# Kernel optimization log

Hardware: AMD Instinct MI355X
Metric: run time of the kernel (lower is better)

Reference implementation:

```python
import jax, jax.numpy as jnp
import numpy as np

NUM_EXPERTS = 8
NUM_FEATURES = 2048


def setup_inputs() -> dict:
    key = jax.random.key(0)
    k1, k2, k3 = jax.random.split(key, 3)
    hidden_states = jax.random.normal(k1, (8192, NUM_FEATURES), dtype=jnp.float32)
    gate_up_proj = jax.random.normal(k2, (NUM_EXPERTS, NUM_FEATURES, 2 * NUM_FEATURES), dtype=jnp.float32)
    down_proj = jax.random.normal(k3, (NUM_EXPERTS, NUM_FEATURES, NUM_FEATURES), dtype=jnp.float32)
    return {"hidden_states": hidden_states, "gate_up_proj": gate_up_proj, "down_proj": down_proj}


def reference(hidden_states, gate_up_proj, down_proj):
    E, D = gate_up_proj.shape[0], gate_up_proj.shape[1]
    # (E, T, D) tokens pre-sorted per expert
    h = hidden_states.reshape(E, -1, D)
    # per-expert batched GEMM: (E, T, 2D)
    gate_up = jnp.einsum('etd,edf->etf', h, gate_up_proj)
    gate, up = gate_up[..., :D], gate_up[..., D:]
    # ReLU-gated activation, then down projection: (E, T, D)
    out = jnp.einsum('etd,edf->etf', up * jax.nn.relu(gate), down_proj)
    return out.reshape(-1, D)
```

## Files before the change

### kernel.cpp

```cpp
#include <hip/hip_runtime.h>
#include <stdint.h>


#define NEXP 8
#define DIM  2048
#define TOK  1024
#define NGU  4096
#define BM   128
#define BN   128
#define BK   32
#define LDST 40

typedef __attribute__((ext_vector_type(8))) short short8;
typedef __attribute__((ext_vector_type(4))) float f32x4;

__device__ __forceinline__ uint32_t pkbf(float lo, float hi) {
  return __builtin_amdgcn_perm(__float_as_uint(hi) + 0x8000u,
                               __float_as_uint(lo) + 0x8000u, 0x07060302u);
}

__device__ __forceinline__ uint16_t bf16_rne(float x) {
  uint32_t u = __float_as_uint(x);
  return (uint16_t)((u + 0x7fffu + ((u >> 16) & 1u)) >> 16);
}

__global__ __launch_bounds__(256, 2) void k_gateup(const float* __restrict__ H,
                                                   const float* __restrict__ W1,
                                                   uint16_t* __restrict__ ACT) {
  __shared__ uint16_t As[BM * LDST];
  __shared__ uint16_t Bg[BN * LDST];
  __shared__ uint16_t Bu[BN * LDST];

  const int tid = threadIdx.x;
  const int e   = blockIdx.z;
  const int m0  = blockIdx.y * BM;
  const int n0  = blockIdx.x * BN;

  const float* hA = H + (size_t)(e * TOK + m0) * DIM;
  const float* wE = W1 + (size_t)e * DIM * NGU;

  const int ar = tid >> 1;
  const int ak = (tid & 1) << 4;
  const float* aptr = hA + (size_t)ar * DIM + ak;
  uint16_t* asw = &As[ar * LDST + ak];

  const int bn = tid & 127;
  const int bk = (tid >> 7) << 4;
  const float* gptr = wE + (size_t)bk * NGU + (n0 + bn);
  const float* uptr = gptr + DIM;
  uint16_t* bgw = &Bg[bn * LDST + bk];
  uint16_t* buw = &Bu[bn * LDST + bk];

  const int lane = tid & 63;
  const int wid  = tid >> 6;
  const int wr = (wid >> 1) << 6;
  const int wc = (wid & 1) << 6;
  const int lm = lane & 15;
  const int qd = lane >> 4;

  f32x4 accg[4][4], accu[4][4];
  const f32x4 zero = {0.f, 0.f, 0.f, 0.f};
#pragma unroll
  for (int i = 0; i < 4; ++i)
#pragma unroll
    for (int j = 0; j < 4; ++j) { accg[i][j] = zero; accu[i][j] = zero; }

  const uint16_t* afr = &As[(wr + lm) * LDST + (qd << 3)];
  const uint16_t* gfr = &Bg[(wc + lm) * LDST + (qd << 3)];
  const uint16_t* ufr = &Bu[(wc + lm) * LDST + (qd << 3)];

  for (int k0 = 0; k0 < DIM; k0 += BK) {
    float4 a0 = *(const float4*)(aptr + 0);
    float4 a1 = *(const float4*)(aptr + 4);
    float4 a2 = *(const float4*)(aptr + 8);
    float4 a3 = *(const float4*)(aptr + 12);
    uint4 aw0 = make_uint4(pkbf(a0.x, a0.y), pkbf(a0.z, a0.w),
                           pkbf(a1.x, a1.y), pkbf(a1.z, a1.w));
    uint4 aw1 = make_uint4(pkbf(a2.x, a2.y), pkbf(a2.z, a2.w),
                           pkbf(a3.x, a3.y), pkbf(a3.z, a3.w));

    float g[16], u[16];
#pragma unroll
    for (int i = 0; i < 16; ++i) g[i] = gptr[(size_t)i * NGU];
#pragma unroll
    for (int i = 0; i < 16; ++i) u[i] = uptr[(size_t)i * NGU];
    uint4 gw0 = make_uint4(pkbf(g[0], g[1]),  pkbf(g[2], g[3]),
                           pkbf(g[4], g[5]),  pkbf(g[6], g[7]));
    uint4 gw1 = make_uint4(pkbf(g[8], g[9]),  pkbf(g[10], g[11]),
                           pkbf(g[12], g[13]), pkbf(g[14], g[15]));
    uint4 uw0 = make_uint4(pkbf(u[0], u[1]),  pkbf(u[2], u[3]),
                           pkbf(u[4], u[5]),  pkbf(u[6], u[7]));
    uint4 uw1 = make_uint4(pkbf(u[8], u[9]),  pkbf(u[10], u[11]),
                           pkbf(u[12], u[13]), pkbf(u[14], u[15]));

    __syncthreads();
    *(uint4*)(asw)     = aw0;
    *(uint4*)(asw + 8) = aw1;
    *(uint4*)(bgw)     = gw0;
    *(uint4*)(bgw + 8) = gw1;
    *(uint4*)(buw)     = uw0;
    *(uint4*)(buw + 8) = uw1;
    __syncthreads();

    short8 a[4], bgf[4], buf[4];
#pragma unroll
    for (int i = 0; i < 4; ++i) a[i] = *(const short8*)(afr + i * 16 * LDST);
#pragma unroll
    for (int j = 0; j < 4; ++j) {
      bgf[j] = *(const short8*)(gfr + j * 16 * LDST);
      buf[j] = *(const short8*)(ufr + j * 16 * LDST);
    }
#pragma unroll
    for (int i = 0; i < 4; ++i)
#pragma unroll
      for (int j = 0; j < 4; ++j) {
        accg[i][j] = __builtin_amdgcn_mfma_f32_16x16x32_bf16(a[i], bgf[j], accg[i][j], 0, 0, 0);
        accu[i][j] = __builtin_amdgcn_mfma_f32_16x16x32_bf16(a[i], buf[j], accu[i][j], 0, 0, 0);
      }

    aptr += BK;
    gptr += (size_t)BK * NGU;
    uptr += (size_t)BK * NGU;
  }

  uint16_t* actE = ACT + (size_t)(e * TOK + m0) * DIM + n0;
#pragma unroll
  for (int i = 0; i < 4; ++i)
#pragma unroll
    for (int j = 0; j < 4; ++j)
#pragma unroll
      for (int t = 0; t < 4; ++t) {
        int row = wr + i * 16 + qd * 4 + t;
        int col = wc + j * 16 + lm;
        float gv = accg[i][j][t];
        float uv = accu[i][j][t];
        actE[(size_t)row * DIM + col] = bf16_rne(uv * fmaxf(gv, 0.f));
      }
}

__global__ __launch_bounds__(256, 3) void k_down(const uint16_t* __restrict__ ACT,
                                                 const float* __restrict__ W2,
                                                 float* __restrict__ OUT) {
  __shared__ uint16_t As[BM * LDST];
  __shared__ uint16_t Bs[BN * LDST];

  const int tid = threadIdx.x;
  const int e   = blockIdx.z;
  const int m0  = blockIdx.y * BM;
  const int n0  = blockIdx.x * BN;

  const uint16_t* aA = ACT + (size_t)(e * TOK + m0) * DIM;
  const float* wE = W2 + (size_t)e * DIM * DIM;

  const int ar = tid >> 1;
  const int ak = (tid & 1) << 4;
  const uint16_t* aptr = aA + (size_t)ar * DIM + ak;
  uint16_t* asw = &As[ar * LDST + ak];

  const int bn = tid & 127;
  const int bk = (tid >> 7) << 4;
  const float* bptr = wE + (size_t)bk * DIM + (n0 + bn);
  uint16_t* bsw = &Bs[bn * LDST + bk];

  const int lane = tid & 63;
  const int wid  = tid >> 6;
  const int wr = (wid >> 1) << 6;
  const int wc = (wid & 1) << 6;
  const int lm = lane & 15;
  const int qd = lane >> 4;

  f32x4 acc[4][4];
  const f32x4 zero = {0.f, 0.f, 0.f, 0.f};
#pragma unroll
  for (int i = 0; i < 4; ++i)
#pragma unroll
    for (int j = 0; j < 4; ++j) acc[i][j] = zero;

  const uint16_t* afr = &As[(wr + lm) * LDST + (qd << 3)];
  const uint16_t* bfr = &Bs[(wc + lm) * LDST + (qd << 3)];

  for (int k0 = 0; k0 < DIM; k0 += BK) {
    uint4 aw0 = *(const uint4*)(aptr);
    uint4 aw1 = *(const uint4*)(aptr + 8);
    float b[16];
#pragma unroll
    for (int i = 0; i < 16; ++i) b[i] = bptr[(size_t)i * DIM];
    uint4 bw0 = make_uint4(pkbf(b[0], b[1]),  pkbf(b[2], b[3]),
                           pkbf(b[4], b[5]),  pkbf(b[6], b[7]));
    uint4 bw1 = make_uint4(pkbf(b[8], b[9]),  pkbf(b[10], b[11]),
                           pkbf(b[12], b[13]), pkbf(b[14], b[15]));

    __syncthreads();
    *(uint4*)(asw)     = aw0;
    *(uint4*)(asw + 8) = aw1;
    *(uint4*)(bsw)     = bw0;
    *(uint4*)(bsw + 8) = bw1;
    __syncthreads();

    short8 a[4], bf[4];
#pragma unroll
    for (int i = 0; i < 4; ++i) a[i] = *(const short8*)(afr + i * 16 * LDST);
#pragma unroll
    for (int j = 0; j < 4; ++j) bf[j] = *(const short8*)(bfr + j * 16 * LDST);
#pragma unroll
    for (int i = 0; i < 4; ++i)
#pragma unroll
      for (int j = 0; j < 4; ++j)
        acc[i][j] = __builtin_amdgcn_mfma_f32_16x16x32_bf16(a[i], bf[j], acc[i][j], 0, 0, 0);

    aptr += BK;
    bptr += (size_t)BK * DIM;
  }

  float* outE = OUT + (size_t)(e * TOK + m0) * DIM + n0;
#pragma unroll
  for (int i = 0; i < 4; ++i)
#pragma unroll
    for (int j = 0; j < 4; ++j)
#pragma unroll
      for (int t = 0; t < 4; ++t) {
        int row = wr + i * 16 + qd * 4 + t;
        int col = wc + j * 16 + lm;
        outE[(size_t)row * DIM + col] = acc[i][j][t];
      }
}

extern "C" void kernel_launch(void* const* d_in, const int* in_sizes, int n_in,
                              void* d_out, int out_size, void* d_ws, size_t ws_size,
                              hipStream_t stream) {
  const float* H  = (const float*)d_in[0];
  const float* W1 = (const float*)d_in[1];
  const float* W2 = (const float*)d_in[2];
  float* OUT = (float*)d_out;
  uint16_t* ACT = (uint16_t*)d_ws;

  dim3 blk(256);
  dim3 g1(DIM / BN, TOK / BM, NEXP);
  k_gateup<<<g1, blk, 0, stream>>>(H, W1, ACT);
  dim3 g2(DIM / BN, TOK / BM, NEXP);
  k_down<<<g2, blk, 0, stream>>>(ACT, W2, OUT);
}
```

Measured before the change: 785.7 us.

## Prefetch next K-tile into registers and load down-proj A fragments directly from global

```diff
diff --git a/kernel.cpp b/kernel.cpp
--- a/kernel.cpp
+++ b/kernel.cpp
@@ -69,21 +69,22 @@
   const uint16_t* gfr = &Bg[(wc + lm) * LDST + (qd << 3)];
   const uint16_t* ufr = &Bu[(wc + lm) * LDST + (qd << 3)];
 
+  float4 a0 = *(const float4*)(aptr + 0);
+  float4 a1 = *(const float4*)(aptr + 4);
+  float4 a2 = *(const float4*)(aptr + 8);
+  float4 a3 = *(const float4*)(aptr + 12);
+  float g[16], u[16];
+#pragma unroll
+  for (int i = 0; i < 16; ++i) g[i] = gptr[(size_t)i * NGU];
+#pragma unroll
+  for (int i = 0; i < 16; ++i) u[i] = uptr[(size_t)i * NGU];
+
+#pragma unroll 1
   for (int k0 = 0; k0 < DIM; k0 += BK) {
-    float4 a0 = *(const float4*)(aptr + 0);
-    float4 a1 = *(const float4*)(aptr + 4);
-    float4 a2 = *(const float4*)(aptr + 8);
-    float4 a3 = *(const float4*)(aptr + 12);
     uint4 aw0 = make_uint4(pkbf(a0.x, a0.y), pkbf(a0.z, a0.w),
                            pkbf(a1.x, a1.y), pkbf(a1.z, a1.w));
     uint4 aw1 = make_uint4(pkbf(a2.x, a2.y), pkbf(a2.z, a2.w),
                            pkbf(a3.x, a3.y), pkbf(a3.z, a3.w));
-
-    float g[16], u[16];
-#pragma unroll
-    for (int i = 0; i < 16; ++i) g[i] = gptr[(size_t)i * NGU];
-#pragma unroll
-    for (int i = 0; i < 16; ++i) u[i] = uptr[(size_t)i * NGU];
     uint4 gw0 = make_uint4(pkbf(g[0], g[1]),  pkbf(g[2], g[3]),
                            pkbf(g[4], g[5]),  pkbf(g[6], g[7]));
     uint4 gw1 = make_uint4(pkbf(g[8], g[9]),  pkbf(g[10], g[11]),
@@ -102,6 +103,20 @@
     *(uint4*)(buw + 8) = uw1;
     __syncthreads();
 
+    aptr += BK;
+    gptr += (size_t)BK * NGU;
+    uptr += (size_t)BK * NGU;
+    if (k0 + BK < DIM) {
+      a0 = *(const float4*)(aptr + 0);
+      a1 = *(const float4*)(aptr + 4);
+      a2 = *(const float4*)(aptr + 8);
+      a3 = *(const float4*)(aptr + 12);
+#pragma unroll
+      for (int i = 0; i < 16; ++i) g[i] = gptr[(size_t)i * NGU];
+#pragma unroll
+      for (int i = 0; i < 16; ++i) u[i] = uptr[(size_t)i * NGU];
+    }
+
     short8 a[4], bgf[4], buf[4];
 #pragma unroll
     for (int i = 0; i < 4; ++i) a[i] = *(const short8*)(afr + i * 16 * LDST);
@@ -117,10 +132,6 @@
         accg[i][j] = __builtin_amdgcn_mfma_f32_16x16x32_bf16(a[i], bgf[j], accg[i][j], 0, 0, 0);
         accu[i][j] = __builtin_amdgcn_mfma_f32_16x16x32_bf16(a[i], buf[j], accu[i][j], 0, 0, 0);
       }
-
-    aptr += BK;
-    gptr += (size_t)BK * NGU;
-    uptr += (size_t)BK * NGU;
   }
 
   uint16_t* actE = ACT + (size_t)(e * TOK + m0) * DIM + n0;
@@ -138,10 +149,9 @@
       }
 }
 
-__global__ __launch_bounds__(256, 3) void k_down(const uint16_t* __restrict__ ACT,
+__global__ __launch_bounds__(256, 2) void k_down(const uint16_t* __restrict__ ACT,
                                                  const float* __restrict__ W2,
                                                  float* __restrict__ OUT) {
-  __shared__ uint16_t As[BM * LDST];
   __shared__ uint16_t Bs[BN * LDST];
 
   const int tid = threadIdx.x;
@@ -151,11 +161,6 @@
 
   const uint16_t* aA = ACT + (size_t)(e * TOK + m0) * DIM;
   const float* wE = W2 + (size_t)e * DIM * DIM;
-
-  const int ar = tid >> 1;
-  const int ak = (tid & 1) << 4;
-  const uint16_t* aptr = aA + (size_t)ar * DIM + ak;
-  uint16_t* asw = &As[ar * LDST + ak];
 
   const int bn = tid & 127;
   const int bk = (tid >> 7) << 4;
@@ -169,6 +174,8 @@
   const int lm = lane & 15;
   const int qd = lane >> 4;
 
+  const uint16_t* agp = aA + (size_t)(wr + lm) * DIM + (qd << 3);
+
   f32x4 acc[4][4];
   const f32x4 zero = {0.f, 0.f, 0.f, 0.f};
 #pragma unroll
@@ -176,30 +183,40 @@
 #pragma unroll
     for (int j = 0; j < 4; ++j) acc[i][j] = zero;
 
-  const uint16_t* afr = &As[(wr + lm) * LDST + (qd << 3)];
   const uint16_t* bfr = &Bs[(wc + lm) * LDST + (qd << 3)];
 
+  short8 an[4];
+#pragma unroll
+  for (int i = 0; i < 4; ++i) an[i] = *(const short8*)(agp + (size_t)i * 16 * DIM);
+  float b[16];
+#pragma unroll
+  for (int i = 0; i < 16; ++i) b[i] = bptr[(size_t)i * DIM];
+
+#pragma unroll 1
   for (int k0 = 0; k0 < DIM; k0 += BK) {
-    uint4 aw0 = *(const uint4*)(aptr);
-    uint4 aw1 = *(const uint4*)(aptr + 8);
-    float b[16];
-#pragma unroll
-    for (int i = 0; i < 16; ++i) b[i] = bptr[(size_t)i * DIM];
     uint4 bw0 = make_uint4(pkbf(b[0], b[1]),  pkbf(b[2], b[3]),
                            pkbf(b[4], b[5]),  pkbf(b[6], b[7]));
     uint4 bw1 = make_uint4(pkbf(b[8], b[9]),  pkbf(b[10], b[11]),
                            pkbf(b[12], b[13]), pkbf(b[14], b[15]));
-
-    __syncthreads();
-    *(uint4*)(asw)     = aw0;
-    *(uint4*)(asw + 8) = aw1;
+    short8 a[4];
+#pragma unroll
+    for (int i = 0; i < 4; ++i) a[i] = an[i];
+
+    __syncthreads();
     *(uint4*)(bsw)     = bw0;
     *(uint4*)(bsw + 8) = bw1;
     __syncthreads();
 
-    short8 a[4], bf[4];
-#pragma unroll
-    for (int i = 0; i < 4; ++i) a[i] = *(const short8*)(afr + i * 16 * LDST);
+    bptr += (size_t)BK * DIM;
+    agp  += BK;
+    if (k0 + BK < DIM) {
+#pragma unroll
+      for (int i = 0; i < 4; ++i) an[i] = *(const short8*)(agp + (size_t)i * 16 * DIM);
+#pragma unroll
+      for (int i = 0; i < 16; ++i) b[i] = bptr[(size_t)i * DIM];
+    }
+
+    short8 bf[4];
 #pragma unroll
     for (int j = 0; j < 4; ++j) bf[j] = *(const short8*)(bfr + j * 16 * LDST);
 #pragma unroll
@@ -207,9 +224,6 @@
 #pragma unroll
       for (int j = 0; j < 4; ++j)
         acc[i][j] = __builtin_amdgcn_mfma_f32_16x16x32_bf16(a[i], bf[j], acc[i][j], 0, 0, 0);
-
-    aptr += BK;
-    bptr += (size_t)BK * DIM;
   }
 
   float* outE = OUT + (size_t)(e * TOK + m0) * DIM + n0;
```

After: 777.8 us. Within noise of the previous version (-1.0%).
